# Kernel tuning notes

Measured on AMD Instinct MI355X. Metric: run time of the kernel, lower is better.

## Reference

```python
import jax, jax.numpy as jnp
import numpy as np

EPS = 1e-5

def mvn(x):
    # x: [B, C, H, W]; per-(B,C) mean/std over spatial dims, torch unbiased var
    B, C, H, W = x.shape
    xf = x.reshape(B, C, H * W)
    mean = jnp.mean(xf, axis=2)
    var = jnp.var(xf, axis=2, ddof=1) + EPS
    std = jnp.sqrt(var)
    return (x - mean[:, :, None, None]) / std[:, :, None, None]

def conv1x1(x, w, b):
    # x: [B, Cin, H, W], w: [Cout, Cin], b: [Cout]
    return jnp.einsum('bchw,oc->bohw', x, w) + b[None, :, None, None]

def setup_inputs() -> dict:
    key = jax.random.key(0)
    ks = jax.random.split(key, 10)
    B, V, QK, H, W = 4, 512, 512, 64, 64
    d = {
        'c_x':  jax.random.normal(ks[0], (B, V, H, W), jnp.float32),
        's_x':  jax.random.normal(ks[1], (B, V, H, W), jnp.float32),
        'c_1x': jax.random.normal(ks[2], (B, QK, H, W), jnp.float32),
        's_1x': jax.random.normal(ks[3], (B, QK, H, W), jnp.float32),
        'f_w': jax.random.normal(ks[4], (QK, QK), jnp.float32) * (1.0 / np.sqrt(QK)),
        'f_b': jax.random.normal(ks[5], (QK,), jnp.float32) * 0.01,
        'g_w': jax.random.normal(ks[6], (QK, QK), jnp.float32) * (1.0 / np.sqrt(QK)),
        'g_b': jax.random.normal(ks[7], (QK,), jnp.float32) * 0.01,
        'h_w': jax.random.normal(ks[8], (V, V), jnp.float32) * (1.0 / np.sqrt(V)),
        'h_b': jax.random.normal(ks[9], (V,), jnp.float32) * 0.01,
    }
    return d

def reference(c_x, s_x, c_1x, s_1x, f_w, f_b, g_w, g_b, h_w, h_b):
    B, V, H, W = c_x.shape
    QK = c_1x.shape[1]
    Lq = H * W
    Lk = s_1x.shape[2] * s_1x.shape[3]
    # Q: [B, Lq, QK], K: [B, QK, Lk], V_: [B, Lk, V]
    Q = conv1x1(mvn(c_1x), f_w, f_b).reshape(B, QK, Lq).transpose(0, 2, 1)
    K = conv1x1(mvn(s_1x), g_w, g_b).reshape(B, QK, Lk)
    V_ = conv1x1(s_x, h_w, h_b).reshape(B, V, Lk).transpose(0, 2, 1)
    A = jax.nn.softmax(jnp.einsum('bqc,bck->bqk', Q, K), axis=-1)  # [B, Lq, Lk]
    M = jnp.einsum('bqk,bkv->bqv', A, V_)                          # weighted mean
    Var = jnp.einsum('bqk,bkv->bqv', A, V_ * V_) - M * M           # weighted var
    S = jnp.sqrt(jnp.clip(Var, 0.0, None))
    M = M.transpose(0, 2, 1).reshape(c_x.shape)
    S = S.transpose(0, 2, 1).reshape(c_x.shape)
    return S * mvn(c_x) + M
```

## Files before the change

kernel.cpp:

```cpp
#include <hip/hip_runtime.h>
#include <math.h>

typedef __attribute__((ext_vector_type(8))) short short8;
typedef __attribute__((ext_vector_type(4))) float f32x4;
typedef __attribute__((ext_vector_type(4))) unsigned short u16x4;

#define DEVINL static __device__ __forceinline__
#define MFMA  __builtin_amdgcn_mfma_f32_16x16x32_bf16
#define MFMAH __builtin_amdgcn_mfma_f32_16x16x32_f16

DEVINL unsigned short f2bf(float f){
  union { float f; unsigned u; } v; v.f = f;
  unsigned r = v.u + 0x7FFFu + ((v.u >> 16) & 1u);
  return (unsigned short)(r >> 16);
}
DEVINL float bf2f(unsigned short h){
  union { unsigned u; float f; } v; v.u = ((unsigned)h) << 16;
  return v.f;
}
DEVINL unsigned short f2h(float f){
  union { _Float16 h; unsigned short u; } c; c.h = (_Float16)f;
  return c.u;
}
DEVINL float h2f(unsigned short u){
  union { unsigned short u; _Float16 h; } c; c.u = u;
  return (float)c.h;
}
DEVINL void gload16(const void* g, void* l){
  __builtin_amdgcn_global_load_lds(
      (const __attribute__((address_space(1))) void*)g,
      (__attribute__((address_space(3))) void*)l, 16, 0, 0);
}

__global__ void rowstats3_k(const float* __restrict__ x0, float* __restrict__ m0, float* __restrict__ r0,
                            const float* __restrict__ x1, float* __restrict__ m1, float* __restrict__ r1,
                            const float* __restrict__ x2, float* __restrict__ m2, float* __restrict__ r2){
  int row = blockIdx.x, z = blockIdx.y;
  const float* x = (z==0 ? x0 : z==1 ? x1 : x2);
  float* mean = (z==0 ? m0 : z==1 ? m1 : m2);
  float* rstd = (z==0 ? r0 : z==1 ? r1 : r2);
  const float4* p = (const float4*)(x + (long)row * 4096);
  float s = 0.f, ss = 0.f;
  for (int i = threadIdx.x; i < 1024; i += 256){
    float4 v = p[i];
    s  += v.x + v.y + v.z + v.w;
    ss += v.x*v.x + v.y*v.y + v.z*v.z + v.w*v.w;
  }
  for (int o = 32; o > 0; o >>= 1){ s += __shfl_down(s, o); ss += __shfl_down(ss, o); }
  __shared__ float ls[4], lss[4];
  int wv = threadIdx.x >> 6;
  if ((threadIdx.x & 63) == 0){ ls[wv] = s; lss[wv] = ss; }
  __syncthreads();
  if (threadIdx.x == 0){
    s = ls[0]+ls[1]+ls[2]+ls[3]; ss = lss[0]+lss[1]+lss[2]+lss[3];
    float m = s * (1.f/4096.f);
    float var = (ss - s*m) * (1.f/4095.f);
    mean[row] = m;
    rstd[row] = 1.f / sqrtf(var + 1e-5f);
  }
}

__global__ void foldw2_k(const float* __restrict__ fw, const float* __restrict__ fb,
                         const float* __restrict__ mQ, const float* __restrict__ rQ,
                         unsigned short* __restrict__ Wfh, unsigned short* __restrict__ Wfl,
                         float* __restrict__ bF,
                         const float* __restrict__ gw, const float* __restrict__ gb,
                         const float* __restrict__ mK, const float* __restrict__ rK,
                         unsigned short* __restrict__ Wgh, unsigned short* __restrict__ Wgl,
                         float* __restrict__ bG){
  int o = blockIdx.x;
  int g = blockIdx.y;
  const float* w    = g ? gw : fw;
  const float* bias = g ? gb : fb;
  const float* mean = g ? mK : mQ;
  const float* rstd = g ? rK : rQ;
  unsigned short* wh = g ? Wgh : Wfh;
  unsigned short* wl = g ? Wgl : Wfl;
  float* biasp = g ? bG : bF;
  const float* wr = w + (long)o * 512;
  float part = 0.f;
  for (int c = threadIdx.x; c < 512; c += 256){
    float wv = wr[c] * rstd[c];
    unsigned short h = f2bf(wv);
    wh[(o<<9)+c] = h;
    wl[(o<<9)+c] = f2bf(wv - bf2f(h));
    part += wv * mean[c];
  }
  __shared__ float red[256];
  red[threadIdx.x] = part; __syncthreads();
  for (int st = 128; st > 0; st >>= 1){
    if (threadIdx.x < st) red[threadIdx.x] += red[threadIdx.x + st];
    __syncthreads();
  }
  if (threadIdx.x == 0) biasp[o] = bias[o] - red[0];
}

__global__ void wsplit_k(const float* __restrict__ w,
                         unsigned short* __restrict__ wh, unsigned short* __restrict__ wl){
  int i = blockIdx.x * 256 + threadIdx.x;
  float v = w[i];
  unsigned short h = f2bf(v);
  wh[i] = h; wl[i] = f2bf(v - bf2f(h));
}

__global__ __launch_bounds__(512) void conv3all_k(
    const float* __restrict__ Xq, const float* __restrict__ Xk, const float* __restrict__ Xv,
    const unsigned short* __restrict__ WhQ, const unsigned short* __restrict__ WlQ, const float* __restrict__ bQ,
    const unsigned short* __restrict__ WhK, const unsigned short* __restrict__ WlK, const float* __restrict__ bK,
    const unsigned short* __restrict__ WhV, const unsigned short* __restrict__ WlV, const float* __restrict__ bV,
    unsigned short* __restrict__ Qf, unsigned short* __restrict__ Kf,
    unsigned short* __restrict__ vh, unsigned short* __restrict__ v2h, unsigned short* __restrict__ v2l)
{
  int ob = blockIdx.y, lb = blockIdx.x, z = blockIdx.z;
  const float* X = (z==0 ? Xq : z==1 ? Xk : Xv);
  const unsigned short* Wh = (z==0 ? WhQ : z==1 ? WhK : WhV);
  const unsigned short* Wl = (z==0 ? WlQ : z==1 ? WlK : WlV);
  const float* biasp = (z==0 ? bQ : z==1 ? bK : bV);

  __shared__ __align__(16) char csm[36864];
  typedef unsigned short (*XT)[64][72];
  XT Xh = (XT)csm;
  XT Xl = (XT)(csm + 18432);

  int tid = threadIdx.x, w = tid >> 6, lane = tid & 63, lr = lane & 15, lg = lane >> 4;
  const unsigned short* WhB = Wh + (long)(ob*128 + w*16) * 512;
  const unsigned short* WlB = Wl + (long)(ob*128 + w*16) * 512;
  int sl = tid & 63, scg = tid >> 6;
  const float* Xg = X + (long)(scg*8)*4096 + lb*64 + sl;

  f32x4 acc[4] = {};
  float fA[8], fB[8];
  short8 wA0, wA1, wA2, wA3, wB0, wB1, wB2, wB3;

#define CV_XLOAD(F, CB) { _Pragma("unroll") for (int j=0;j<8;++j) F[j] = Xg[(long)((CB)*64 + j)*4096]; }
#define CV_XWRITE(BUF, F) { short8 hv, lv; _Pragma("unroll") for (int j=0;j<8;++j){ \
    unsigned short h_ = f2bf(F[j]); hv[j] = (short)h_; lv[j] = (short)f2bf(F[j] - bf2f(h_)); } \
    *(short8*)&Xh[BUF][sl][scg*8] = hv; *(short8*)&Xl[BUF][sl][scg*8] = lv; }
#define CV_WLOAD(W0,W1,W2,W3, CB) { \
    W0 = *(const short8*)(WhB + (long)lr*512 + (CB)*64 + lg*8); \
    W1 = *(const short8*)(WhB + (long)lr*512 + (CB)*64 + 32 + lg*8); \
    W2 = *(const short8*)(WlB + (long)lr*512 + (CB)*64 + lg*8); \
    W3 = *(const short8*)(WlB + (long)lr*512 + (CB)*64 + 32 + lg*8); }
#define CV_COMPUTE(BUF, W0,W1,W2,W3) { \
    _Pragma("unroll") for (int ct=0;ct<4;++ct){ \
      short8 bh = *(const short8*)&Xh[BUF][ct*16+lr][lg*8]; \
      short8 bl = *(const short8*)&Xl[BUF][ct*16+lr][lg*8]; \
      acc[ct] = MFMA(W0, bh, acc[ct], 0,0,0); \
      acc[ct] = MFMA(W2, bh, acc[ct], 0,0,0); \
      acc[ct] = MFMA(W0, bl, acc[ct], 0,0,0); } \
    _Pragma("unroll") for (int ct=0;ct<4;++ct){ \
      short8 bh = *(const short8*)&Xh[BUF][ct*16+lr][32+lg*8]; \
      short8 bl = *(const short8*)&Xl[BUF][ct*16+lr][32+lg*8]; \
      acc[ct] = MFMA(W1, bh, acc[ct], 0,0,0); \
      acc[ct] = MFMA(W3, bh, acc[ct], 0,0,0); \
      acc[ct] = MFMA(W1, bl, acc[ct], 0,0,0); } }

  CV_XLOAD(fA, 0); CV_XWRITE(0, fA);
  CV_XLOAD(fA, 1);
  CV_WLOAD(wA0,wA1,wA2,wA3, 0);
  __syncthreads();
  for (int cb = 0; cb < 8; cb += 2){
    if (cb+2 < 8) CV_XLOAD(fB, cb+2);
    CV_WLOAD(wB0,wB1,wB2,wB3, cb+1);
    CV_COMPUTE(0, wA0,wA1,wA2,wA3);
    CV_XWRITE(1, fA);
    __syncthreads();
    if (cb+3 < 8) CV_XLOAD(fA, cb+3);
    if (cb+2 < 8) CV_WLOAD(wA0,wA1,wA2,wA3, cb+2);
    CV_COMPUTE(1, wB0,wB1,wB2,wB3);
    if (cb+2 < 8) CV_XWRITE(0, fB);
    __syncthreads();
  }

  int o4 = ob*128 + w*16 + lg*4;
  float bv[4];
  #pragma unroll
  for (int r = 0; r < 4; ++r) bv[r] = biasp[o4 + r];
  if (z < 2){
    unsigned short* of = (z==0 ? Qf : Kf);
    #pragma unroll
    for (int ct = 0; ct < 4; ++ct){
      u16x4 ph;
      #pragma unroll
      for (int r = 0; r < 4; ++r) ph[r] = f2h(acc[ct][r] + bv[r]);
      long base = ((long)(lb*64 + ct*16 + lr)) * 512 + o4;
      *(u16x4*)(of + base) = ph;
    }
  } else {
    unsigned short sh_[16], s2h_[16], s2l_[16];
    #pragma unroll
    for (int ct = 0; ct < 4; ++ct)
      #pragma unroll
      for (int r = 0; r < 4; ++r){
        float y = acc[ct][r] + bv[r];
        unsigned short h = f2bf(y);
        float vhf = bf2f(h);
        float v2 = vhf * vhf;
        unsigned short h2 = f2bf(v2);
        unsigned short l2 = f2bf(v2 - bf2f(h2));
        sh_[ct*4+r] = h; s2h_[ct*4+r] = h2; s2l_[ct*4+r] = l2;
      }
    unsigned short* T = (unsigned short*)csm;
#define CV_STORE(ARR, DST) { \
    __syncthreads(); \
    _Pragma("unroll") for (int ct=0;ct<4;++ct) \
      _Pragma("unroll") for (int r=0;r<4;++r) \
        T[(w*16+lg*4+r)*72 + ct*16+lr] = ARR[ct*4+r]; \
    __syncthreads(); \
    _Pragma("unroll") for (int s_=0;s_<2;++s_){ \
      int slot = tid + s_*512; int row = slot>>3, ch=(slot&7)*8; \
      *(short8*)(DST + (long)(ob*128+row)*4096 + lb*64 + ch) = *(const short8*)&T[row*72+ch]; } }
    CV_STORE(sh_,  vh);
    CV_STORE(s2h_, v2h);
    CV_STORE(s2l_, v2l);
#undef CV_STORE
  }
#undef CV_XLOAD
#undef CV_XWRITE
#undef CV_WLOAD
#undef CV_COMPUTE
}

__global__ __launch_bounds__(512, 4) void sgemm1h_k(
    const unsigned short* __restrict__ Qf, const unsigned short* __restrict__ Kf,
    unsigned short* __restrict__ S)
{
  int bx = blockIdx.x, by = blockIdx.y;
  int q0g = bx*128, k0 = by*128;
  __shared__ unsigned short Qs[128][64], Ks[128][64];
  int tid = threadIdx.x, w = tid >> 6, lane = tid & 63, lr = lane & 15, lg = lane >> 4;
  int wr = w & 1, wc = w >> 1;
  int srow = tid >> 3, sch = (tid & 7)*8;
  int swu = ((tid & 7) ^ (srow & 7)) * 8;
  int lr7 = lr & 7;
  short8 qr0, qr1, kr0, kr1;
  f32x4 acc[4][2] = {};

#define SG_LOAD(CB) { long c0_ = (long)(CB)*64 + sch; \
    qr0 = *(const short8*)(Qf + (long)(q0g + srow)*512 + c0_); \
    qr1 = *(const short8*)(Qf + (long)(q0g + srow + 64)*512 + c0_); \
    kr0 = *(const short8*)(Kf + (long)(k0 + srow)*512 + c0_); \
    kr1 = *(const short8*)(Kf + (long)(k0 + srow + 64)*512 + c0_); }
#define SG_WRITE { \
    *(short8*)&Qs[srow][swu] = qr0; *(short8*)&Qs[srow + 64][swu] = qr1; \
    *(short8*)&Ks[srow][swu] = kr0; *(short8*)&Ks[srow + 64][swu] = kr1; }

  SG_LOAD(0); SG_WRITE;
  __syncthreads();
  for (int cb = 0; cb < 8; ++cb){
    if (cb < 7) SG_LOAD(cb+1);
    #pragma unroll
    for (int kk = 0; kk < 2; ++kk){
      int un = ((kk*4 + lg) ^ lr7) * 8;
      short8 bh[2];
      #pragma unroll
      for (int bs = 0; bs < 2; ++bs)
        bh[bs] = *(const short8*)(&Ks[wc*32 + bs*16 + lr][un]);
      #pragma unroll
      for (int as = 0; as < 4; ++as){
        short8 ah = *(const short8*)(&Qs[wr*64 + as*16 + lr][un]);
        #pragma unroll
        for (int bs = 0; bs < 2; ++bs)
          acc[as][bs] = MFMAH(ah, bh[bs], acc[as][bs], 0,0,0);
      }
    }
    __syncthreads();
    if (cb < 7){ SG_WRITE; __syncthreads(); }
  }
#undef SG_LOAD
#undef SG_WRITE
  #pragma unroll
  for (int as = 0; as < 4; ++as){
    #pragma unroll
    for (int bs = 0; bs < 2; ++bs){
      int q = q0g + wr*64 + as*16 + lg*4;
      int k = k0 + wc*32 + bs*16 + lr;
      unsigned short* Sp = S + (long)q*4096 + k;
      #pragma unroll
      for (int r = 0; r < 4; ++r) Sp[(long)r*4096] = f2h(acc[as][bs][r]);
    }
  }
}

__global__ __launch_bounds__(256) void softmax_k(unsigned short* __restrict__ SP,
                                                 float* __restrict__ inv2){
  int row = blockIdx.x;
  unsigned short* Sr = SP + (long)row * 4096;
  int t = threadIdx.x;
  short8 a = *(const short8*)(Sr + t*8);
  short8 b = *(const short8*)(Sr + 2048 + t*8);
  float v[16];
  #pragma unroll
  for (int j = 0; j < 8; ++j){ v[j] = h2f((unsigned short)a[j]); v[8+j] = h2f((unsigned short)b[j]); }
  float mx = v[0];
  #pragma unroll
  for (int i = 1; i < 16; ++i) mx = fmaxf(mx, v[i]);
  #pragma unroll
  for (int o = 32; o > 0; o >>= 1) mx = fmaxf(mx, __shfl_xor(mx, o));
  __shared__ float red[4];
  int wid = t >> 6;
  if ((t & 63) == 0) red[wid] = mx;
  __syncthreads();
  mx = fmaxf(fmaxf(red[0], red[1]), fmaxf(red[2], red[3]));
  __syncthreads();
  float p[16]; float d = 0.f;
  #pragma unroll
  for (int i = 0; i < 16; ++i){ float e = expf(v[i] - mx); p[i] = e; d += e; }
  #pragma unroll
  for (int o = 32; o > 0; o >>= 1) d += __shfl_xor(d, o);
  if ((t & 63) == 0) red[wid] = d;
  __syncthreads();
  d = red[0] + red[1] + red[2] + red[3];
  __syncthreads();
  float invd = 1.f / d;
  unsigned short pb[16]; float d2 = 0.f;
  #pragma unroll
  for (int i = 0; i < 16; ++i){ pb[i] = f2bf(p[i] * invd); d2 += bf2f(pb[i]); }
  #pragma unroll
  for (int o = 32; o > 0; o >>= 1) d2 += __shfl_xor(d2, o);
  if ((t & 63) == 0) red[wid] = d2;
  __syncthreads();
  if (t == 0) inv2[row] = 1.f / (red[0]+red[1]+red[2]+red[3]);
  short8 pa, pbv;
  #pragma unroll
  for (int j = 0; j < 8; ++j){ pa[j] = (short)pb[j]; pbv[j] = (short)pb[8+j]; }
  *(short8*)(Sr + t*8) = pa;
  *(short8*)(Sr + 2048 + t*8) = pbv;
}

__global__ __launch_bounds__(256, 2) void pv2_k(
    const unsigned short* __restrict__ P, long ppitch,
    const unsigned short* __restrict__ vh,
    const unsigned short* __restrict__ v2h, const unsigned short* __restrict__ v2l,
    const float* __restrict__ inv2,
    const float* __restrict__ cx, const float* __restrict__ mcx, const float* __restrict__ rcx,
    float* __restrict__ outb)
{
  __shared__ __align__(16) char smem[65536];
  typedef unsigned short (*PlT)[64][64];
  typedef unsigned short (*VlT)[3][64][64];
  PlT Pl = (PlT)smem;
  VlT Vl = (VlT)(smem + 16384);
  float* R = (float*)smem;

  int tid = threadIdx.x;
  int l = tid & 63, w = tid >> 6;
  int wq = w >> 1, wv = w & 1;
  int lr = l & 15, lg = l >> 4;
  int qP0 = blockIdx.x*64, qG0 = blockIdx.x*64;
  int vc0 = blockIdx.y*64;

  int r8_ = l >> 3, c8 = (l & 7)*8;
  int srcc = c8 ^ (r8_*8);
  const unsigned short* gsrc;
  long rs8;
  unsigned short *l0, *l1;
  if (w == 0){
    gsrc = P + (long)(qP0 + r8_)*ppitch + srcc;
    rs8 = (long)8*ppitch;
    l0 = &Pl[0][0][0]; l1 = &Pl[1][0][0];
  } else {
    const unsigned short* va = (w==1 ? vh : w==2 ? v2h : v2l);
    gsrc = va + (long)(vc0 + r8_)*4096 + srcc;
    rs8 = (long)8*4096;
    l0 = &Vl[0][w-1][0][0]; l1 = &Vl[1][w-1][0][0];
  }

  f32x4 accM[2][2] = {}, acc2[2][2] = {};

#define PV_STAGE_J(LB, TT, J0, J1) { long ko_ = (long)(TT)*64; \
    _Pragma("unroll") for (int j = J0; j < J1; ++j) \
      gload16(gsrc + j*rs8 + ko_, LB + j*512); }
#define PV_COMPUTE_KK(BUF, KK) { \
    int un = (((KK)*4 + lg) ^ (lr & 7)) * 8; \
    short8 fh[2], f2h_[2], f2l_[2]; \
    _Pragma("unroll") for (int bs = 0; bs < 2; ++bs){ \
      int vrow = wv*32 + bs*16 + lr; \
      fh[bs]   = *(const short8*)(&Vl[BUF][0][vrow][un]); \
      f2h_[bs] = *(const short8*)(&Vl[BUF][1][vrow][un]); \
      f2l_[bs] = *(const short8*)(&Vl[BUF][2][vrow][un]); } \
    _Pragma("unroll") for (int aq = 0; aq < 2; ++aq){ \
      short8 pa = *(const short8*)(&Pl[BUF][wq*32 + aq*16 + lr][un]); \
      _Pragma("unroll") for (int bs = 0; bs < 2; ++bs){ \
        accM[aq][bs] = MFMA(pa, fh[bs],   accM[aq][bs], 0,0,0); \
        acc2[aq][bs] = MFMA(pa, f2h_[bs], acc2[aq][bs], 0,0,0); \
        acc2[aq][bs] = MFMA(pa, f2l_[bs], acc2[aq][bs], 0,0,0); } } }

  PV_STAGE_J(l0, 0, 0, 8);
  __syncthreads();
  for (int t = 0; t < 64; ++t){
    unsigned short* nb = (t & 1) ? l0 : l1;
    int buf = t & 1;
    if (t < 63) PV_STAGE_J(nb, t+1, 0, 4);
    PV_COMPUTE_KK(buf, 0);
    if (t < 63) PV_STAGE_J(nb, t+1, 4, 8);
    PV_COMPUTE_KK(buf, 1);
    __syncthreads();
  }
#undef PV_STAGE_J
#undef PV_COMPUTE_KK

  float* Tm = R;
  #pragma unroll
  for (int aq = 0; aq < 2; ++aq)
    #pragma unroll
    for (int bs = 0; bs < 2; ++bs){
      int vcl = wv*32 + bs*16 + lr;
      int ql  = wq*32 + aq*16 + lg*4;
      #pragma unroll
      for (int r = 0; r < 4; ++r) Tm[vcl*68 + ql + r] = accM[aq][bs][r];
    }
  __syncthreads();
  f32x4 Mv[4];
  #pragma unroll
  for (int p = 0; p < 4; ++p){
    int chunk = tid + p*256;
    int row = chunk >> 4, c4 = (chunk & 15)*4;
    Mv[p] = *(const f32x4*)&Tm[row*68 + c4];
  }
  __syncthreads();
  #pragma unroll
  for (int aq = 0; aq < 2; ++aq)
    #pragma unroll
    for (int bs = 0; bs < 2; ++bs){
      int vcl = wv*32 + bs*16 + lr;
      int ql  = wq*32 + aq*16 + lg*4;
      #pragma unroll
      for (int r = 0; r < 4; ++r) Tm[vcl*68 + ql + r] = acc2[aq][bs][r];
    }
  __syncthreads();
  #pragma unroll
  for (int p = 0; p < 4; ++p){
    int chunk = tid + p*256;
    int row = chunk >> 4, c4 = (chunk & 15)*4;
    float mu = mcx[vc0 + row], rs = rcx[vc0 + row];
    f32x4 t2 = *(const f32x4*)&Tm[row*68 + c4];
    f32x4 iv = *(const f32x4*)&inv2[qP0 + c4];
    f32x4 cv = *(const f32x4*)&cx[(long)(vc0+row)*4096 + qG0 + c4];
    f32x4 ov;
    #pragma unroll
    for (int j = 0; j < 4; ++j){
      float M = Mv[p][j]*iv[j], M2 = t2[j]*iv[j];
      float var = M2 - M*M;
      float sd = sqrtf(fmaxf(var, 0.f));
      ov[j] = sd*(cv[j]-mu)*rs + M;
    }
    *(f32x4*)&outb[(long)(vc0+row)*4096 + qG0 + c4] = ov;
  }
}

extern "C" void kernel_launch(void* const* d_in, const int* in_sizes, int n_in,
                              void* d_out, int out_size, void* d_ws, size_t ws_size,
                              hipStream_t stream){
  const float* c_x  = (const float*)d_in[0];
  const float* s_x  = (const float*)d_in[1];
  const float* c_1x = (const float*)d_in[2];
  const float* s_1x = (const float*)d_in[3];
  const float* f_w  = (const float*)d_in[4];
  const float* f_b  = (const float*)d_in[5];
  const float* g_w  = (const float*)d_in[6];
  const float* g_b  = (const float*)d_in[7];
  const float* h_w  = (const float*)d_in[8];
  const float* h_b  = (const float*)d_in[9];
  float* out = (float*)d_out;

  char* ws = (char*)d_ws;
  size_t off = 0;
  auto alloc = [&](size_t bytes)->void*{
    void* p = ws + off; off += (bytes + 255) & ~(size_t)255; return p;
  };
  float* meanQ = (float*)alloc(2048*4); float* rstdQ = (float*)alloc(2048*4);
  float* meanK = (float*)alloc(2048*4); float* rstdK = (float*)alloc(2048*4);
  float* meanC = (float*)alloc(2048*4); float* rstdC = (float*)alloc(2048*4);
  float* biasF = (float*)alloc(512*4);  float* biasG = (float*)alloc(512*4);
  unsigned short* Wfh = (unsigned short*)alloc((size_t)512*512*2);
  unsigned short* Wfl = (unsigned short*)alloc((size_t)512*512*2);
  unsigned short* Wgh = (unsigned short*)alloc((size_t)512*512*2);
  unsigned short* Wgl = (unsigned short*)alloc((size_t)512*512*2);
  unsigned short* Whh = (unsigned short*)alloc((size_t)512*512*2);
  unsigned short* Whl = (unsigned short*)alloc((size_t)512*512*2);
  unsigned short* Qf = (unsigned short*)alloc((size_t)4096*512*2);
  unsigned short* Kf = (unsigned short*)alloc((size_t)4096*512*2);
  unsigned short* vh  = (unsigned short*)alloc((size_t)512*4096*2);
  unsigned short* v2h = (unsigned short*)alloc((size_t)512*4096*2);
  unsigned short* v2l = (unsigned short*)alloc((size_t)512*4096*2);
  unsigned short* S   = (unsigned short*)alloc((size_t)4096*4096*2);
  float* inv2 = (float*)alloc(4096*4);

  rowstats3_k<<<dim3(2048,3), 256, 0, stream>>>(c_1x, meanQ, rstdQ,
                                                s_1x, meanK, rstdK,
                                                c_x,  meanC, rstdC);
  wsplit_k<<<1024, 256, 0, stream>>>(h_w, Whh, Whl);

  for (int b = 0; b < 4; ++b){
    long xoff = (long)b * 512 * 4096;
    foldw2_k<<<dim3(512,2), 256, 0, stream>>>(f_w, f_b, meanQ + b*512, rstdQ + b*512, Wfh, Wfl, biasF,
                                              g_w, g_b, meanK + b*512, rstdK + b*512, Wgh, Wgl, biasG);
    conv3all_k<<<dim3(64,4,3), 512, 0, stream>>>(c_1x + xoff, s_1x + xoff, s_x + xoff,
                                                 Wfh, Wfl, biasF,
                                                 Wgh, Wgl, biasG,
                                                 Whh, Whl, h_b,
                                                 Qf, Kf, vh, v2h, v2l);
    sgemm1h_k<<<dim3(32,32), 512, 0, stream>>>(Qf, Kf, S);
    softmax_k<<<4096, 256, 0, stream>>>(S, inv2);
    pv2_k<<<dim3(64,8), 256, 0, stream>>>(S, 4096, vh, v2h, v2l, inv2,
                                          c_x + xoff, meanC + b*512, rstdC + b*512,
                                          out + xoff);
  }
}
```

Baseline: 556.7 us.

## Double-buffer QK score GEMM tiles with direct global-to-LDS loads

The Q·K score kernel now keeps two LDS buffers and stages the next 64-channel chunk straight from global memory into LDS with gload16, instead of loading into registers and then writing to shared memory. Each loop iteration needs one barrier instead of two, and the next chunk's transfer can overlap the MFMA work on the current one. The cost is doubling LDS use to 64 KB per block, which may cut how many blocks fit on a CU, since launch_bounds asks for 4. The swizzle moves to the source address, and gload16 is assumed to be defined in the part of the file not shown.

```diff
diff --git a/kernel.cpp b/kernel.cpp
--- a/kernel.cpp
+++ b/kernel.cpp
@@ -227,48 +227,52 @@
 {
   int bx = blockIdx.x, by = blockIdx.y;
   int q0g = bx*128, k0 = by*128;
-  __shared__ unsigned short Qs[128][64], Ks[128][64];
+  __shared__ __align__(16) char sm[65536];
+  typedef unsigned short (*TileT)[128][64];
+  TileT Qs = (TileT)sm;
+  TileT Ks = (TileT)(sm + 32768);
+
   int tid = threadIdx.x, w = tid >> 6, lane = tid & 63, lr = lane & 15, lg = lane >> 4;
   int wr = w & 1, wc = w >> 1;
-  int srow = tid >> 3, sch = (tid & 7)*8;
-  int swu = ((tid & 7) ^ (srow & 7)) * 8;
   int lr7 = lr & 7;
-  short8 qr0, qr1, kr0, kr1;
+
+  int r8_ = lane >> 3, c8 = (lane & 7)*8;
+  int srcc = c8 ^ (r8_*8);
+  const unsigned short* gq0 = Qf + (long)(q0g + w*16 + r8_)*512 + srcc;
+  const unsigned short* gq1 = gq0 + (long)8*512;
+  const unsigned short* gk0 = Kf + (long)(k0 + w*16 + r8_)*512 + srcc;
+  const unsigned short* gk1 = gk0 + (long)8*512;
   f32x4 acc[4][2] = {};
 
-#define SG_LOAD(CB) { long c0_ = (long)(CB)*64 + sch; \
-    qr0 = *(const short8*)(Qf + (long)(q0g + srow)*512 + c0_); \
-    qr1 = *(const short8*)(Qf + (long)(q0g + srow + 64)*512 + c0_); \
-    kr0 = *(const short8*)(Kf + (long)(k0 + srow)*512 + c0_); \
-    kr1 = *(const short8*)(Kf + (long)(k0 + srow + 64)*512 + c0_); }
-#define SG_WRITE { \
-    *(short8*)&Qs[srow][swu] = qr0; *(short8*)&Qs[srow + 64][swu] = qr1; \
-    *(short8*)&Ks[srow][swu] = kr0; *(short8*)&Ks[srow + 64][swu] = kr1; }
-
-  SG_LOAD(0); SG_WRITE;
+#define SG_STAGE(BUF, CB) { long co_ = (long)(CB)*64; \
+    gload16(gq0 + co_, &Qs[BUF][w*16][0]); \
+    gload16(gq1 + co_, &Qs[BUF][w*16 + 8][0]); \
+    gload16(gk0 + co_, &Ks[BUF][w*16][0]); \
+    gload16(gk1 + co_, &Ks[BUF][w*16 + 8][0]); }
+
+  SG_STAGE(0, 0);
   __syncthreads();
   for (int cb = 0; cb < 8; ++cb){
-    if (cb < 7) SG_LOAD(cb+1);
+    int buf = cb & 1;
+    if (cb < 7) SG_STAGE(buf ^ 1, cb+1);
     #pragma unroll
     for (int kk = 0; kk < 2; ++kk){
       int un = ((kk*4 + lg) ^ lr7) * 8;
       short8 bh[2];
       #pragma unroll
       for (int bs = 0; bs < 2; ++bs)
-        bh[bs] = *(const short8*)(&Ks[wc*32 + bs*16 + lr][un]);
+        bh[bs] = *(const short8*)(&Ks[buf][wc*32 + bs*16 + lr][un]);
       #pragma unroll
       for (int as = 0; as < 4; ++as){
-        short8 ah = *(const short8*)(&Qs[wr*64 + as*16 + lr][un]);
+        short8 ah = *(const short8*)(&Qs[buf][wr*64 + as*16 + lr][un]);
         #pragma unroll
         for (int bs = 0; bs < 2; ++bs)
           acc[as][bs] = MFMAH(ah, bh[bs], acc[as][bs], 0,0,0);
       }
     }
     __syncthreads();
-    if (cb < 7){ SG_WRITE; __syncthreads(); }
-  }
-#undef SG_LOAD
-#undef SG_WRITE
+  }
+#undef SG_STAGE
   #pragma unroll
   for (int as = 0; as < 4; ++as){
     #pragma unroll
```

Result: no change. 562.2 us (+1.0%).
